# Performance work log

Measured on AMD Instinct MI355X. Metric: run time of the kernel, lower is better.

## Reference

```python
import jax, jax.numpy as jnp
import numpy as np

L = 2
NB = (L + 1) ** 2      # 9 spherical-harmonic basis components
C = 256                # in_channels == out_channels
MID = C // 4           # 64, mid_channels in the FF
N = 4096               # nodes
K = 16                 # neighbors (neighbor_cg)


def _real_sh_l2(rel):
    # Real spherical harmonics up to l=2 of normalized edge directions. rel: [N,K,3] -> [N,K,9]
    r = jnp.sqrt(jnp.sum(rel * rel, axis=-1, keepdims=True))
    d = rel / (r + 1e-8)
    x, y, z = d[..., 0], d[..., 1], d[..., 2]
    c0 = 0.28209479177387814
    c1 = 0.4886025119029199
    c2 = 1.0925484305920792
    c2b = 0.31539156525252005
    c2c = 0.5462742152960396
    return jnp.stack([
        jnp.full_like(x, c0),
        c1 * y, c1 * z, c1 * x,
        c2 * x * y, c2 * y * z, c2b * (3.0 * z * z - 1.0), c2 * x * z, c2c * (x * x - y * y),
    ], axis=-1)


def setup_inputs() -> dict:
    key = jax.random.key(0)
    ks = jax.random.split(key, 8)
    return {
        "s_feats": jax.random.normal(ks[0], (N, NB, C), jnp.float32),
        "s_points": jax.random.normal(ks[1], (N, 3), jnp.float32),
        "cg": jax.random.normal(ks[2], (NB, NB, NB), jnp.float32) * 0.1,  # CG coefficient buffer
        "W_proj": jax.random.normal(ks[3], (C, C), jnp.float32) / np.sqrt(C),
        "ln_w": jnp.ones((L + 1, C), jnp.float32),
        "ln_b": jnp.zeros((C,), jnp.float32),
        "W_ff1": jax.random.normal(ks[4], (C, MID), jnp.float32) / np.sqrt(C),
        "W_gate": jax.random.normal(ks[5], (MID, MID * (L + 1)), jnp.float32) / np.sqrt(MID),
        "W_ff2": jax.random.normal(ks[6], (MID, C), jnp.float32) / np.sqrt(MID),
        "neighbor_indices": jax.random.randint(ks[7], (N, K), 0, N),
    }


def _forward(s_feats, s_points, cg, W_proj, ln_w, ln_b, W_ff1, W_gate, W_ff2, neighbor_indices):
    # --- CGConv: project, gather neighbors, SH of edge directions, CG tensor product, mean-aggregate ---
    h = jnp.einsum('nic,co->nio', s_feats, W_proj)               # [N,9,C]
    nbr = h[neighbor_indices]                                    # [N,K,9,C] irregular gather
    rel = s_points[neighbor_indices] - s_points[:, None, :]      # [N,K,3]
    sh = _real_sh_l2(rel)                                        # [N,K,9]
    x = jnp.einsum('nkic,nkj,ijo->noc', nbr, sh, cg) / K         # [N,9,C]
    # --- residual add of input (linear3 == Identity since in_channels == out_channels) ---
    x = x + s_feats
    shortcut = x
    # --- EquivariantLayerNormV2: per-degree RMS norm; mean-center + bias only on l=0 ---
    outs = []
    for l in range(L + 1):
        f = x[:, l * l:(l + 1) * (l + 1), :]                     # [N,2l+1,C]
        if l == 0:
            f = f - jnp.mean(f, axis=-1, keepdims=True)
        nrm = jnp.mean(f * f, axis=(1, 2), keepdims=True)
        f = f * jax.lax.rsqrt(nrm + 1e-5) * ln_w[l][None, None, :]
        if l == 0:
            f = f + ln_b[None, None, :]
        outs.append(f)
    y = jnp.concatenate(outs, axis=1)
    # --- FF: Linear -> Gate_3j -> Linear, residual ---
    z = jnp.einsum('nic,cm->nim', y, W_ff1)                      # [N,9,MID]
    after = z[:, 0, :] @ W_gate                                  # [N, MID*(L+1)]
    t0 = jax.nn.silu(after[:, :MID])
    mult = jax.nn.sigmoid(after[:, MID:])                        # [N, MID*L]
    gated = [t0[:, None, :]]
    for l in range(1, L + 1):
        gated.append(z[:, l * l:(l + 1) * (l + 1), :] * mult[:, None, (l - 1) * MID:l * MID])
    z = jnp.concatenate(gated, axis=1)                           # [N,9,MID]
    return jnp.einsum('nim,mc->nic', z, W_ff2) + shortcut


def reference(s_feats, s_points, cg, W_proj, ln_w, ln_b, W_ff1, W_gate, W_ff2, neighbor_indices):
    return _forward(s_feats, s_points, cg, W_proj, ln_w, ln_b, W_ff1, W_gate, W_ff2, neighbor_indices)
```

## Files before the change

kernel.cpp:

```cpp
#include <hip/hip_runtime.h>
#include <hip/hip_bf16.h>

#define N_PTS  4096
#define NB     9
#define C      256
#define MID    64
#define KNBR   16
#define NROWS  (N_PTS * NB)

typedef __attribute__((ext_vector_type(8))) short          short8;
typedef __attribute__((ext_vector_type(4))) float          f32x4;
typedef __attribute__((ext_vector_type(4))) unsigned short ush4;
typedef __attribute__((ext_vector_type(8))) unsigned short ush8;

static __device__ __forceinline__ unsigned short f2bf(float f) {
    union { __hip_bfloat16 h; unsigned short u; } cv;
    cv.h = __float2bfloat16(f);
    return cv.u;
}
static __device__ __forceinline__ float bf2f(unsigned short s) {
    union { unsigned u; float f; } v; v.u = ((unsigned)s) << 16;
    return v.f;
}
static __device__ __forceinline__ unsigned packbf(float a, float b) {
    return (unsigned)f2bf(a) | ((unsigned)f2bf(b) << 16);
}

#define LDK 40
__global__ __launch_bounds__(256) void k_proj(const float* __restrict__ A,
                                              const float* __restrict__ W,
                                              unsigned short* __restrict__ H) {
    __shared__ unsigned short As[128 * LDK];
    __shared__ unsigned short Bs[128 * LDK];
    const int tid = threadIdx.x;
    const int r0  = blockIdx.x * 128;
    const int n0  = blockIdx.y * 128;
    const int wave = tid >> 6, lane = tid & 63;
    const int wm = wave >> 1, wn = wave & 1;
    const int lr = lane & 15, lg = lane >> 4;

    f32x4 acc[4][4];
#pragma unroll
    for (int a = 0; a < 4; ++a)
#pragma unroll
        for (int b = 0; b < 4; ++b) acc[a][b] = (f32x4){0.f, 0.f, 0.f, 0.f};

    for (int k0 = 0; k0 < C; k0 += 32) {
        __syncthreads();
#pragma unroll
        for (int rep = 0; rep < 4; ++rep) {
            const int e   = rep * 256 + tid;
            const int row = e >> 3;
            const int c4  = (e & 7) << 2;
            const float4 v = *reinterpret_cast<const float4*>(&A[(size_t)(r0 + row) * C + k0 + c4]);
            ush4 s = { f2bf(v.x), f2bf(v.y), f2bf(v.z), f2bf(v.w) };
            *reinterpret_cast<ush4*>(&As[row * LDK + c4]) = s;
        }
#pragma unroll
        for (int rep = 0; rep < 4; ++rep) {
            const int e = rep * 256 + tid;
            const int k = e >> 5;
            const int j = (e & 31) << 2;
            const float4 v = *reinterpret_cast<const float4*>(&W[(size_t)(k0 + k) * C + n0 + j]);
            Bs[(j + 0) * LDK + k] = f2bf(v.x);
            Bs[(j + 1) * LDK + k] = f2bf(v.y);
            Bs[(j + 2) * LDK + k] = f2bf(v.z);
            Bs[(j + 3) * LDK + k] = f2bf(v.w);
        }
        __syncthreads();

        short8 af[4], bfr[4];
#pragma unroll
        for (int mf = 0; mf < 4; ++mf)
            af[mf] = *reinterpret_cast<const short8*>(&As[(wm * 64 + mf * 16 + lr) * LDK + lg * 8]);
#pragma unroll
        for (int nf = 0; nf < 4; ++nf)
            bfr[nf] = *reinterpret_cast<const short8*>(&Bs[(wn * 64 + nf * 16 + lr) * LDK + lg * 8]);
#pragma unroll
        for (int mf = 0; mf < 4; ++mf)
#pragma unroll
            for (int nf = 0; nf < 4; ++nf)
                acc[mf][nf] = __builtin_amdgcn_mfma_f32_16x16x32_bf16(af[mf], bfr[nf], acc[mf][nf], 0, 0, 0);
    }
#pragma unroll
    for (int mf = 0; mf < 4; ++mf)
#pragma unroll
        for (int nf = 0; nf < 4; ++nf) {
            const int col = n0 + wn * 64 + nf * 16 + lr;
#pragma unroll
            for (int r = 0; r < 4; ++r) {
                const int row = r0 + wm * 64 + mf * 16 + lg * 4 + r;
                H[(size_t)row * C + col] = f2bf(acc[mf][nf][r]);
            }
        }
}

__global__ __launch_bounds__(256) void k_cg_ln(const unsigned short* __restrict__ Hb,
                                               const float* __restrict__ s_feats,
                                               const float* __restrict__ pts,
                                               const float* __restrict__ cg,
                                               const int*   __restrict__ nbr,
                                               const float* __restrict__ ln_w,
                                               const float* __restrict__ ln_b,
                                               unsigned short* __restrict__ Xb,
                                               unsigned short* __restrict__ Yb) {
    __shared__ unsigned short Bs[256 * 40];
    __shared__ unsigned short wT[16 * 168];
    __shared__ float cg_s[729];
    __shared__ float sh_s[KNBR][NB];
    __shared__ int   idx_s[KNBR];
    __shared__ float red_s[2][4];

    const int tid  = threadIdx.x;
    const int n    = blockIdx.x;
    const int wv   = tid >> 6;
    const int lane = tid & 63;
    const int g16  = lane >> 4;
    const int l16  = lane & 15;

    {
        unsigned* w32 = reinterpret_cast<unsigned*>(wT);
        for (int e = tid; e < (16 * 168) / 2; e += 256) w32[e] = 0u;
    }
    for (int e = tid; e < 729; e += 256) cg_s[e] = cg[e];
    if (tid < KNBR) {
        const int idx = nbr[n * KNBR + tid];
        idx_s[tid] = idx;
        const float px = pts[idx * 3 + 0] - pts[n * 3 + 0];
        const float py = pts[idx * 3 + 1] - pts[n * 3 + 1];
        const float pz = pts[idx * 3 + 2] - pts[n * 3 + 2];
        const float r  = sqrtf(px * px + py * py + pz * pz);
        const float iv = 1.f / (r + 1e-8f);
        const float dx = px * iv, dy = py * iv, dz = pz * iv;
        const float c1 = 0.4886025119029199f;
        const float c2 = 1.0925484305920792f;
        sh_s[tid][0] = 0.28209479177387814f;
        sh_s[tid][1] = c1 * dy;
        sh_s[tid][2] = c1 * dz;
        sh_s[tid][3] = c1 * dx;
        sh_s[tid][4] = c2 * dx * dy;
        sh_s[tid][5] = c2 * dy * dz;
        sh_s[tid][6] = 0.31539156525252005f * (3.f * dz * dz - 1.f);
        sh_s[tid][7] = c2 * dx * dz;
        sh_s[tid][8] = 0.5462742152960396f * (dx * dx - dy * dy);
    }
    __syncthreads();

    for (int t = tid; t < 144 * 9; t += 256) {
        const int ki = t / 9;
        const int o  = t - ki * 9;
        const int kk = ki / 9;
        const int ii = ki - kk * 9;
        float s = 0.f;
#pragma unroll
        for (int j = 0; j < 9; ++j) s = fmaf(sh_s[kk][j], cg_s[ii * 81 + j * 9 + o], s);
        wT[o * 168 + ki] = f2bf(s);
    }

    const int r = tid & 31;
    const int s = tid >> 5;

    f32x4 acc[4];
#pragma unroll
    for (int i = 0; i < 4; ++i) acc[i] = (f32x4){0.f, 0.f, 0.f, 0.f};

    for (int cc = 0; cc < 5; ++cc) {
        const int nrows = (cc == 4) ? 16 : 32;
        ush8 q[4];
        if (r < nrows) {
            const int ki = cc * 32 + r;
            const int kk = ki / 9;
            const int ii = ki - kk * 9;
            const unsigned short* hrow = Hb + (size_t)(idx_s[kk] * NB + ii) * C + s * 32;
#pragma unroll
            for (int u = 0; u < 4; ++u)
                q[u] = *reinterpret_cast<const ush8*>(hrow + u * 8);
        }
        __syncthreads();
        if (r < nrows) {
#pragma unroll
            for (int u = 0; u < 4; ++u) {
                const unsigned short* qe = reinterpret_cast<const unsigned short*>(&q[u]);
#pragma unroll
                for (int e = 0; e < 8; ++e)
                    Bs[(s * 32 + u * 8 + e) * 40 + r] = qe[e];
            }
        }
        __syncthreads();

        const short8 af = *reinterpret_cast<const short8*>(&wT[l16 * 168 + cc * 32 + g16 * 8]);
        short8 bfr[4];
#pragma unroll
        for (int ti = 0; ti < 4; ++ti)
            bfr[ti] = *reinterpret_cast<const short8*>(&Bs[(wv * 64 + ti * 16 + l16) * 40 + g16 * 8]);
#pragma unroll
        for (int ti = 0; ti < 4; ++ti)
            acc[ti] = __builtin_amdgcn_mfma_f32_16x16x32_bf16(af, bfr[ti], acc[ti], 0, 0, 0);
    }

    __syncthreads();
    float* const Dld = reinterpret_cast<float*>(Bs);
#pragma unroll
    for (int ti = 0; ti < 4; ++ti) {
        const int cgl = (wv * 4 + ti) * 16 + l16;
#pragma unroll
        for (int rr = 0; rr < 4; ++rr) {
            const int o = g16 * 4 + rr;
            if (o < 9) Dld[o * 264 + cgl] = acc[ti][rr] * (1.f / (float)KNBR);
        }
    }
    __syncthreads();

    float2 xv[9];
    float s0 = 0.f, s1 = 0.f, s2 = 0.f, s3 = 0.f;
    if (tid < 128) {
        const int c = tid * 2;
        const float* sf = s_feats + (size_t)n * (NB * C) + c;
#pragma unroll
        for (int i = 0; i < 9; ++i) {
            const float2 d = *reinterpret_cast<const float2*>(&Dld[i * 264 + c]);
            const float2 sv = *reinterpret_cast<const float2*>(&sf[(size_t)i * C]);
            xv[i].x = d.x + sv.x;
            xv[i].y = d.y + sv.y;
        }
        s0 = xv[0].x + xv[0].y;
        s1 = xv[0].x * xv[0].x + xv[0].y * xv[0].y;
#pragma unroll
        for (int o = 1; o < 4; ++o) s2 += xv[o].x * xv[o].x + xv[o].y * xv[o].y;
#pragma unroll
        for (int o = 4; o < 9; ++o) s3 += xv[o].x * xv[o].x + xv[o].y * xv[o].y;
#pragma unroll
        for (int off = 32; off >= 1; off >>= 1) {
            s0 += __shfl_xor(s0, off);
            s1 += __shfl_xor(s1, off);
            s2 += __shfl_xor(s2, off);
            s3 += __shfl_xor(s3, off);
        }
        if (lane == 0) {
            red_s[wv][0] = s0; red_s[wv][1] = s1;
            red_s[wv][2] = s2; red_s[wv][3] = s3;
        }
    }
    __syncthreads();
    if (tid < 128) {
        s0 = red_s[0][0] + red_s[1][0];
        s1 = red_s[0][1] + red_s[1][1];
        s2 = red_s[0][2] + red_s[1][2];
        s3 = red_s[0][3] + red_s[1][3];

        const float mean0 = s0 * (1.f / 256.f);
        const float nrm0  = s1 * (1.f / 256.f) - mean0 * mean0;
        const float nrm1  = s2 * (1.f / 768.f);
        const float nrm2  = s3 * (1.f / 1280.f);
        const float r0v = rsqrtf(nrm0 + 1e-5f);
        const float r1v = rsqrtf(nrm1 + 1e-5f);
        const float r2v = rsqrtf(nrm2 + 1e-5f);

        const int c = tid * 2;
        const float2 lw0 = *reinterpret_cast<const float2*>(ln_w + c);
        const float2 lw1 = *reinterpret_cast<const float2*>(ln_w + C + c);
        const float2 lw2 = *reinterpret_cast<const float2*>(ln_w + 2 * C + c);
        const float2 lb0 = *reinterpret_cast<const float2*>(ln_b + c);

        unsigned* xo = reinterpret_cast<unsigned*>(Xb + (size_t)n * (NB * C));
        unsigned* yo = reinterpret_cast<unsigned*>(Yb + (size_t)n * (NB * C));
#pragma unroll
        for (int i = 0; i < 9; ++i) xo[i * 128 + tid] = packbf(xv[i].x, xv[i].y);
        yo[tid] = packbf((xv[0].x - mean0) * r0v * lw0.x + lb0.x,
                         (xv[0].y - mean0) * r0v * lw0.y + lb0.y);
#pragma unroll
        for (int i = 1; i < 4; ++i)
            yo[i * 128 + tid] = packbf(xv[i].x * r1v * lw1.x, xv[i].y * r1v * lw1.y);
#pragma unroll
        for (int i = 4; i < 9; ++i)
            yo[i * 128 + tid] = packbf(xv[i].x * r2v * lw2.x, xv[i].y * r2v * lw2.y);
    }
}

__global__ __launch_bounds__(256) void k_ff1(const unsigned short* __restrict__ Yb,
                                             const float* __restrict__ W1,
                                             unsigned short* __restrict__ Zb) {
    __shared__ unsigned short As[128 * LDK];
    __shared__ unsigned short Bs[64 * LDK];
    const int tid = threadIdx.x;
    const int r0  = blockIdx.x * 128;
    const int wave = tid >> 6, lane = tid & 63;
    const int wm = wave >> 1, wn = wave & 1;
    const int lr = lane & 15, lg = lane >> 4;

    f32x4 acc[4][2];
#pragma unroll
    for (int a = 0; a < 4; ++a) { acc[a][0] = (f32x4){0.f,0.f,0.f,0.f}; acc[a][1] = (f32x4){0.f,0.f,0.f,0.f}; }

    for (int k0 = 0; k0 < C; k0 += 32) {
        __syncthreads();
#pragma unroll
        for (int rep = 0; rep < 4; ++rep) {
            const int e   = rep * 256 + tid;
            const int row = e >> 3;
            const int c4  = (e & 7) << 2;
            ush4 s = *reinterpret_cast<const ush4*>(&Yb[(size_t)(r0 + row) * C + k0 + c4]);
            *reinterpret_cast<ush4*>(&As[row * LDK + c4]) = s;
        }
#pragma unroll
        for (int rep = 0; rep < 2; ++rep) {
            const int e = rep * 256 + tid;
            const int k = e >> 4;
            const int j = (e & 15) << 2;
            const float4 v = *reinterpret_cast<const float4*>(&W1[(size_t)(k0 + k) * MID + j]);
            Bs[(j + 0) * LDK + k] = f2bf(v.x);
            Bs[(j + 1) * LDK + k] = f2bf(v.y);
            Bs[(j + 2) * LDK + k] = f2bf(v.z);
            Bs[(j + 3) * LDK + k] = f2bf(v.w);
        }
        __syncthreads();

        short8 af[4], bfr[2];
#pragma unroll
        for (int mf = 0; mf < 4; ++mf)
            af[mf] = *reinterpret_cast<const short8*>(&As[(wm * 64 + mf * 16 + lr) * LDK + lg * 8]);
#pragma unroll
        for (int nf = 0; nf < 2; ++nf)
            bfr[nf] = *reinterpret_cast<const short8*>(&Bs[(wn * 32 + nf * 16 + lr) * LDK + lg * 8]);
#pragma unroll
        for (int mf = 0; mf < 4; ++mf)
#pragma unroll
            for (int nf = 0; nf < 2; ++nf)
                acc[mf][nf] = __builtin_amdgcn_mfma_f32_16x16x32_bf16(af[mf], bfr[nf], acc[mf][nf], 0, 0, 0);
    }
#pragma unroll
    for (int mf = 0; mf < 4; ++mf)
#pragma unroll
        for (int nf = 0; nf < 2; ++nf) {
            const int col = wn * 32 + nf * 16 + lr;
#pragma unroll
            for (int r = 0; r < 4; ++r) {
                const int row = r0 + wm * 64 + mf * 16 + lg * 4 + r;
                Zb[(size_t)row * MID + col] = f2bf(acc[mf][nf][r]);
            }
        }
}

__global__ __launch_bounds__(192) void k_gate(const unsigned short* __restrict__ Zb,
                                              const float* __restrict__ Wg,
                                              float* __restrict__ G) {
    __shared__ float wgs[64 * 192];
    __shared__ float z0s[16 * 64];
    const int tid = threadIdx.x;
    const int n0  = blockIdx.x * 16;

    for (int e = tid; e < 64 * 192; e += 192) wgs[e] = Wg[e];
    for (int e = tid; e < 16 * 64; e += 192) {
        const int r = e >> 6, m = e & 63;
        z0s[e] = bf2f(Zb[(size_t)(n0 + r) * (NB * MID) + m]);
    }
    __syncthreads();

    const int j = tid;
    for (int r = 0; r < 16; ++r) {
        float acc = 0.f;
        for (int m0 = 0; m0 < 64; m0 += 4) {
            const float4 zv = *reinterpret_cast<const float4*>(&z0s[r * 64 + m0]);
            acc = fmaf(zv.x, wgs[(m0 + 0) * 192 + j], acc);
            acc = fmaf(zv.y, wgs[(m0 + 1) * 192 + j], acc);
            acc = fmaf(zv.z, wgs[(m0 + 2) * 192 + j], acc);
            acc = fmaf(zv.w, wgs[(m0 + 3) * 192 + j], acc);
        }
        const float sig = 1.f / (1.f + expf(-acc));
        G[(size_t)(n0 + r) * 192 + j] = (j < 64) ? acc * sig : sig;
    }
}

#define LDK64 72
__global__ __launch_bounds__(256) void k_final(const unsigned short* __restrict__ Zb,
                                               const float* __restrict__ G,
                                               const float* __restrict__ W2,
                                               const unsigned short* __restrict__ Xb,
                                               float* __restrict__ OUT) {
    __shared__ unsigned short As[128 * LDK64];
    __shared__ unsigned short Bs[128 * LDK64];
    const int tid = threadIdx.x;
    const int r0  = blockIdx.x * 128;
    const int n0  = blockIdx.y * 128;
    const int wave = tid >> 6, lane = tid & 63;
    const int wm = wave >> 1, wn = wave & 1;
    const int lr = lane & 15, lg = lane >> 4;

    {
        const int arow = tid >> 1;
        const int kh   = (tid & 1) * 32;
        const int grow = r0 + arow;
        const int nn   = grow / 9;
        const int ii   = grow - nn * 9;
        if (ii == 0) {
            const float* gp = &G[(size_t)nn * 192 + kh];
#pragma unroll
            for (int j = 0; j < 32; j += 4) {
                const float4 g = *reinterpret_cast<const float4*>(&gp[j]);
                ush4 s = { f2bf(g.x), f2bf(g.y), f2bf(g.z), f2bf(g.w) };
                *reinterpret_cast<ush4*>(&As[arow * LDK64 + kh + j]) = s;
            }
        } else {
            const float* gm = &G[(size_t)nn * 192 + ((ii < 4) ? 64 : 128) + kh];
            const unsigned short* zr = &Zb[(size_t)nn * (NB * MID) + ii * MID + kh];
#pragma unroll
            for (int j = 0; j < 32; j += 4) {
                const ush4 zv = *reinterpret_cast<const ush4*>(&zr[j]);
                const float4 g = *reinterpret_cast<const float4*>(&gm[j]);
                ush4 s = { f2bf(bf2f(zv.x) * g.x), f2bf(bf2f(zv.y) * g.y),
                           f2bf(bf2f(zv.z) * g.z), f2bf(bf2f(zv.w) * g.w) };
                *reinterpret_cast<ush4*>(&As[arow * LDK64 + kh + j]) = s;
            }
        }
    }
#pragma unroll
    for (int rep = 0; rep < 8; ++rep) {
        const int e = rep * 256 + tid;
        const int k = e >> 5;
        const int j = (e & 31) << 2;
        const float4 v = *reinterpret_cast<const float4*>(&W2[(size_t)k * C + n0 + j]);
        Bs[(j + 0) * LDK64 + k] = f2bf(v.x);
        Bs[(j + 1) * LDK64 + k] = f2bf(v.y);
        Bs[(j + 2) * LDK64 + k] = f2bf(v.z);
        Bs[(j + 3) * LDK64 + k] = f2bf(v.w);
    }
    __syncthreads();

    f32x4 acc[4][4];
#pragma unroll
    for (int a = 0; a < 4; ++a)
#pragma unroll
        for (int b = 0; b < 4; ++b) acc[a][b] = (f32x4){0.f, 0.f, 0.f, 0.f};

#pragma unroll
    for (int ks = 0; ks < 2; ++ks) {
        short8 af[4], bfr[4];
#pragma unroll
        for (int mf = 0; mf < 4; ++mf)
            af[mf] = *reinterpret_cast<const short8*>(&As[(wm * 64 + mf * 16 + lr) * LDK64 + ks * 32 + lg * 8]);
#pragma unroll
        for (int nf = 0; nf < 4; ++nf)
            bfr[nf] = *reinterpret_cast<const short8*>(&Bs[(wn * 64 + nf * 16 + lr) * LDK64 + ks * 32 + lg * 8]);
#pragma unroll
        for (int mf = 0; mf < 4; ++mf)
#pragma unroll
            for (int nf = 0; nf < 4; ++nf)
                acc[mf][nf] = __builtin_amdgcn_mfma_f32_16x16x32_bf16(af[mf], bfr[nf], acc[mf][nf], 0, 0, 0);
    }

#pragma unroll
    for (int mf = 0; mf < 4; ++mf)
#pragma unroll
        for (int nf = 0; nf < 4; ++nf) {
            const int col = n0 + wn * 64 + nf * 16 + lr;
#pragma unroll
            for (int r = 0; r < 4; ++r) {
                const int row = r0 + wm * 64 + mf * 16 + lg * 4 + r;
                OUT[(size_t)row * C + col] = acc[mf][nf][r] + bf2f(Xb[(size_t)row * C + col]);
            }
        }
}

extern "C" void kernel_launch(void* const* d_in, const int* in_sizes, int n_in,
                              void* d_out, int out_size, void* d_ws, size_t ws_size,
                              hipStream_t stream) {
    const float* s_feats = (const float*)d_in[0];
    const float* s_pts   = (const float*)d_in[1];
    const float* cg      = (const float*)d_in[2];
    const float* W_proj  = (const float*)d_in[3];
    const float* ln_w    = (const float*)d_in[4];
    const float* ln_b    = (const float*)d_in[5];
    const float* W_ff1   = (const float*)d_in[6];
    const float* W_gate  = (const float*)d_in[7];
    const float* W_ff2   = (const float*)d_in[8];
    const int*   nbr     = (const int*)d_in[9];
    float* out = (float*)d_out;

    unsigned short* Hb = (unsigned short*)d_ws;
    unsigned short* Xb = Hb + (size_t)NROWS * C;
    unsigned short* Yb = Xb + (size_t)NROWS * C;
    unsigned short* Zb = Yb + (size_t)NROWS * C;
    float* G = (float*)(Zb + (size_t)NROWS * MID);

    k_proj  <<<dim3(NROWS / 128, 2), 256, 0, stream>>>(s_feats, W_proj, Hb);
    k_cg_ln <<<N_PTS,                256, 0, stream>>>(Hb, s_feats, s_pts, cg, nbr, ln_w, ln_b, Xb, Yb);
    k_ff1   <<<NROWS / 128,          256, 0, stream>>>(Yb, W_ff1, Zb);
    k_gate  <<<N_PTS / 16,           192, 0, stream>>>(Zb, W_gate, G);
    k_final <<<dim3(NROWS / 128, 2), 256, 0, stream>>>(Zb, G, W_ff2, Xb, out);
}
```

Baseline: 131.9 us.

## Software-pipeline neighbor row gathers and alias CG coefficients into the staging buffer

The cg_ln kernel now issues the first chunk's neighbor-row gather before building the wT weight table, and prefetches the next chunk's rows into registers while the current chunk is written to shared memory and consumed by MFMA. The CG coefficient array no longer has its own shared-memory allocation and instead lives in the Bs staging buffer, lowering LDS use per block and possibly raising occupancy. The aim is to hide global gather latency behind compute. The cost is more live registers and a layout that depends on barrier ordering between the wT build and the first Bs write.

```diff
diff --git a/kernel.cpp b/kernel.cpp
--- a/kernel.cpp
+++ b/kernel.cpp
@@ -106,10 +106,11 @@
                                                unsigned short* __restrict__ Yb) {
     __shared__ unsigned short Bs[256 * 40];
     __shared__ unsigned short wT[16 * 168];
-    __shared__ float cg_s[729];
     __shared__ float sh_s[KNBR][NB];
     __shared__ int   idx_s[KNBR];
     __shared__ float red_s[2][4];
+
+    float* const cg_s = reinterpret_cast<float*>(Bs);
 
     const int tid  = threadIdx.x;
     const int n    = blockIdx.x;
@@ -146,19 +147,31 @@
     }
     __syncthreads();
 
+    const int r = tid & 31;
+    const int s = tid >> 5;
+
+    ush8 q0, q1, q2, q3;
+    {
+        const int ki = r;
+        const int kk = ki / 9;
+        const int ii = ki - kk * 9;
+        const unsigned short* hrow = Hb + (size_t)(idx_s[kk] * NB + ii) * C + s * 32;
+        q0 = *reinterpret_cast<const ush8*>(hrow + 0);
+        q1 = *reinterpret_cast<const ush8*>(hrow + 8);
+        q2 = *reinterpret_cast<const ush8*>(hrow + 16);
+        q3 = *reinterpret_cast<const ush8*>(hrow + 24);
+    }
+
     for (int t = tid; t < 144 * 9; t += 256) {
         const int ki = t / 9;
         const int o  = t - ki * 9;
         const int kk = ki / 9;
         const int ii = ki - kk * 9;
-        float s = 0.f;
-#pragma unroll
-        for (int j = 0; j < 9; ++j) s = fmaf(sh_s[kk][j], cg_s[ii * 81 + j * 9 + o], s);
-        wT[o * 168 + ki] = f2bf(s);
-    }
-
-    const int r = tid & 31;
-    const int s = tid >> 5;
+        float sv = 0.f;
+#pragma unroll
+        for (int j = 0; j < 9; ++j) sv = fmaf(sh_s[kk][j], cg_s[ii * 81 + j * 9 + o], sv);
+        wT[o * 168 + ki] = f2bf(sv);
+    }
 
     f32x4 acc[4];
 #pragma unroll
@@ -166,26 +179,39 @@
 
     for (int cc = 0; cc < 5; ++cc) {
         const int nrows = (cc == 4) ? 16 : 32;
-        ush8 q[4];
+
+        __syncthreads();
+
         if (r < nrows) {
-            const int ki = cc * 32 + r;
-            const int kk = ki / 9;
-            const int ii = ki - kk * 9;
-            const unsigned short* hrow = Hb + (size_t)(idx_s[kk] * NB + ii) * C + s * 32;
-#pragma unroll
-            for (int u = 0; u < 4; ++u)
-                q[u] = *reinterpret_cast<const ush8*>(hrow + u * 8);
-        }
-        __syncthreads();
-        if (r < nrows) {
-#pragma unroll
-            for (int u = 0; u < 4; ++u) {
-                const unsigned short* qe = reinterpret_cast<const unsigned short*>(&q[u]);
-#pragma unroll
-                for (int e = 0; e < 8; ++e)
-                    Bs[(s * 32 + u * 8 + e) * 40 + r] = qe[e];
+            const unsigned short* qe;
+            qe = reinterpret_cast<const unsigned short*>(&q0);
+#pragma unroll
+            for (int e = 0; e < 8; ++e) Bs[(s * 32 + 0 * 8 + e) * 40 + r] = qe[e];
+            qe = reinterpret_cast<const unsigned short*>(&q1);
+#pragma unroll
+            for (int e = 0; e < 8; ++e) Bs[(s * 32 + 1 * 8 + e) * 40 + r] = qe[e];
+            qe = reinterpret_cast<const unsigned short*>(&q2);
+#pragma unroll
+            for (int e = 0; e < 8; ++e) Bs[(s * 32 + 2 * 8 + e) * 40 + r] = qe[e];
+            qe = reinterpret_cast<const unsigned short*>(&q3);
+#pragma unroll
+            for (int e = 0; e < 8; ++e) Bs[(s * 32 + 3 * 8 + e) * 40 + r] = qe[e];
+        }
+
+        if (cc < 4) {
+            const int kin   = (cc + 1) * 32 + r;
+            const bool vldn = (kin < 144);
+            if (vldn) {
+                const int kk = kin / 9;
+                const int ii = kin - kk * 9;
+                const unsigned short* hrow = Hb + (size_t)(idx_s[kk] * NB + ii) * C + s * 32;
+                q0 = *reinterpret_cast<const ush8*>(hrow + 0);
+                q1 = *reinterpret_cast<const ush8*>(hrow + 8);
+                q2 = *reinterpret_cast<const ush8*>(hrow + 16);
+                q3 = *reinterpret_cast<const ush8*>(hrow + 24);
             }
         }
+
         __syncthreads();
 
         const short8 af = *reinterpret_cast<const short8*>(&wT[l16 * 168 + cc * 32 + g16 * 8]);
@@ -218,7 +244,7 @@
         const float* sf = s_feats + (size_t)n * (NB * C) + c;
 #pragma unroll
         for (int i = 0; i < 9; ++i) {
-            const float2 d = *reinterpret_cast<const float2*>(&Dld[i * 264 + c]);
+            const float2 d  = *reinterpret_cast<const float2*>(&Dld[i * 264 + c]);
             const float2 sv = *reinterpret_cast<const float2*>(&sf[(size_t)i * C]);
             xv[i].x = d.x + sv.x;
             xv[i].y = d.y + sv.y;
```

Measured after the change: 129.4 us. About the same (-1.9%).

## Split CG kernel by channel halves, precompute edge weights, fold layernorm into FF1

Applied to the files above, without the earlier changes.

The per-node CG-weight construction moves into a separate kernel that writes a bf16 weight matrix per node. The CG conv is split over two channel halves per node, and all neighbor rows are gathered in one pass into an XOR-swizzled LDS tile instead of a five-step load/sync loop. The layernorm is no longer a separate Y buffer: partial sums go to a scratch array and FF1 applies the normalization while loading X. This aims to raise parallelism, cut synchronizations and drop one full-size intermediate write and read, at the cost of an extra launch, a weight buffer round trip and recomputed norm statistics in FF1.

```diff
diff --git a/kernel.cpp b/kernel.cpp
--- a/kernel.cpp
+++ b/kernel.cpp
@@ -95,37 +95,18 @@
         }
 }
 
-__global__ __launch_bounds__(256) void k_cg_ln(const unsigned short* __restrict__ Hb,
-                                               const float* __restrict__ s_feats,
-                                               const float* __restrict__ pts,
-                                               const float* __restrict__ cg,
-                                               const int*   __restrict__ nbr,
-                                               const float* __restrict__ ln_w,
-                                               const float* __restrict__ ln_b,
-                                               unsigned short* __restrict__ Xb,
-                                               unsigned short* __restrict__ Yb) {
-    __shared__ unsigned short Bs[256 * 40];
-    __shared__ unsigned short wT[16 * 168];
+__global__ __launch_bounds__(256) void k_w(const float* __restrict__ pts,
+                                           const float* __restrict__ cg,
+                                           const int*   __restrict__ nbr,
+                                           unsigned short* __restrict__ w_all) {
     __shared__ float cg_s[729];
     __shared__ float sh_s[KNBR][NB];
-    __shared__ int   idx_s[KNBR];
-    __shared__ float red_s[2][4];
-
-    const int tid  = threadIdx.x;
-    const int n    = blockIdx.x;
-    const int wv   = tid >> 6;
-    const int lane = tid & 63;
-    const int g16  = lane >> 4;
-    const int l16  = lane & 15;
-
-    {
-        unsigned* w32 = reinterpret_cast<unsigned*>(wT);
-        for (int e = tid; e < (16 * 168) / 2; e += 256) w32[e] = 0u;
-    }
+    const int tid = threadIdx.x;
+    const int n   = blockIdx.x;
+
     for (int e = tid; e < 729; e += 256) cg_s[e] = cg[e];
     if (tid < KNBR) {
         const int idx = nbr[n * KNBR + tid];
-        idx_s[tid] = idx;
         const float px = pts[idx * 3 + 0] - pts[n * 3 + 0];
         const float py = pts[idx * 3 + 1] - pts[n * 3 + 1];
         const float pz = pts[idx * 3 + 2] - pts[n * 3 + 2];
@@ -146,85 +127,120 @@
     }
     __syncthreads();
 
-    for (int t = tid; t < 144 * 9; t += 256) {
-        const int ki = t / 9;
-        const int o  = t - ki * 9;
-        const int kk = ki / 9;
-        const int ii = ki - kk * 9;
+#pragma unroll
+    for (int it = 0; it < 10; ++it) {
+        const int t  = it * 256 + tid;
+        const int o  = t / 160;
+        const int ki = t - o * 160;
         float s = 0.f;
-#pragma unroll
-        for (int j = 0; j < 9; ++j) s = fmaf(sh_s[kk][j], cg_s[ii * 81 + j * 9 + o], s);
-        wT[o * 168 + ki] = f2bf(s);
-    }
-
-    const int r = tid & 31;
-    const int s = tid >> 5;
-
-    f32x4 acc[4];
-#pragma unroll
-    for (int i = 0; i < 4; ++i) acc[i] = (f32x4){0.f, 0.f, 0.f, 0.f};
-
-    for (int cc = 0; cc < 5; ++cc) {
-        const int nrows = (cc == 4) ? 16 : 32;
-        ush8 q[4];
-        if (r < nrows) {
-            const int ki = cc * 32 + r;
+        if (o < 9 && ki < 144) {
             const int kk = ki / 9;
             const int ii = ki - kk * 9;
-            const unsigned short* hrow = Hb + (size_t)(idx_s[kk] * NB + ii) * C + s * 32;
-#pragma unroll
-            for (int u = 0; u < 4; ++u)
-                q[u] = *reinterpret_cast<const ush8*>(hrow + u * 8);
-        }
-        __syncthreads();
-        if (r < nrows) {
-#pragma unroll
-            for (int u = 0; u < 4; ++u) {
-                const unsigned short* qe = reinterpret_cast<const unsigned short*>(&q[u]);
-#pragma unroll
-                for (int e = 0; e < 8; ++e)
-                    Bs[(s * 32 + u * 8 + e) * 40 + r] = qe[e];
-            }
-        }
-        __syncthreads();
-
-        const short8 af = *reinterpret_cast<const short8*>(&wT[l16 * 168 + cc * 32 + g16 * 8]);
-        short8 bfr[4];
-#pragma unroll
-        for (int ti = 0; ti < 4; ++ti)
-            bfr[ti] = *reinterpret_cast<const short8*>(&Bs[(wv * 64 + ti * 16 + l16) * 40 + g16 * 8]);
-#pragma unroll
-        for (int ti = 0; ti < 4; ++ti)
-            acc[ti] = __builtin_amdgcn_mfma_f32_16x16x32_bf16(af, bfr[ti], acc[ti], 0, 0, 0);
+#pragma unroll
+            for (int j = 0; j < 9; ++j) s = fmaf(sh_s[kk][j], cg_s[ii * 81 + j * 9 + o], s);
+        }
+        w_all[(size_t)n * 2560 + t] = f2bf(s);
+    }
+}
+
+__global__ __launch_bounds__(256) void k_cg(const unsigned short* __restrict__ Hb,
+                                            const float* __restrict__ s_feats,
+                                            const unsigned short* __restrict__ w_all,
+                                            const int*   __restrict__ nbr,
+                                            unsigned short* __restrict__ Xb,
+                                            float* __restrict__ scr) {
+    __shared__ unsigned short Bs[128 * 168];
+    __shared__ unsigned short wTl[16 * 168];
+    __shared__ int idx_s[KNBR];
+
+    const int tid  = threadIdx.x;
+    const int bid  = blockIdx.x;
+    const int n    = bid >> 1;
+    const int half = bid & 1;
+    const int c0   = half * 128;
+    const int wv   = tid >> 6;
+    const int lane = tid & 63;
+    const int g16  = lane >> 4;
+    const int l16  = lane & 15;
+
+    if (tid < KNBR) idx_s[tid] = nbr[n * KNBR + tid];
+    __syncthreads();
+
+    const int cseg = tid & 15;
+    const int kk   = tid >> 4;
+    const unsigned short* hb = Hb + (size_t)idx_s[kk] * (NB * C) + c0 + cseg * 8;
+    ush8 q[9];
+#pragma unroll
+    for (int j = 0; j < 9; ++j)
+        q[j] = *reinterpret_cast<const ush8*>(hb + (size_t)j * C);
+
+    {
+        const int u  = tid;
+        const int o  = u / 20, p = u - o * 20;
+        const ush8 wv8 = *reinterpret_cast<const ush8*>(w_all + (size_t)n * 2560 + o * 160 + p * 8);
+        *reinterpret_cast<ush8*>(&wTl[o * 168 + p * 8]) = wv8;
+        if (tid < 64) {
+            const int u2 = 256 + tid;
+            const int o2 = u2 / 20, p2 = u2 - o2 * 20;
+            const ush8 w2 = *reinterpret_cast<const ush8*>(w_all + (size_t)n * 2560 + o2 * 160 + p2 * 8);
+            *reinterpret_cast<ush8*>(&wTl[o2 * 168 + p2 * 8]) = w2;
+        }
+    }
+    if (tid < 128) {
+        const ush8 z = (ush8){0, 0, 0, 0, 0, 0, 0, 0};
+        *reinterpret_cast<ush8*>(&Bs[tid * 168 + 144]) = z;
+        *reinterpret_cast<ush8*>(&Bs[tid * 168 + 152]) = z;
+        *reinterpret_cast<ush8*>(&Bs[tid * 168 + 160]) = z;
+    }
+#pragma unroll
+    for (int j = 0; j < 9; ++j) {
+        const unsigned short* qe = reinterpret_cast<const unsigned short*>(&q[j]);
+        const int colk = kk * 9 + j;
+#pragma unroll
+        for (int e = 0; e < 8; ++e) {
+            const int ee = e ^ (cseg & 7);
+            Bs[(cseg * 8 + ee) * 168 + colk] = qe[ee];
+        }
+    }
+    __syncthreads();
+
+    f32x4 acc[2];
+    acc[0] = (f32x4){0.f, 0.f, 0.f, 0.f};
+    acc[1] = (f32x4){0.f, 0.f, 0.f, 0.f};
+#pragma unroll
+    for (int cc = 0; cc < 5; ++cc) {
+        const short8 af = *reinterpret_cast<const short8*>(&wTl[l16 * 168 + cc * 32 + g16 * 8]);
+        const short8 b0 = *reinterpret_cast<const short8*>(&Bs[(wv * 32 + l16) * 168 + cc * 32 + g16 * 8]);
+        const short8 b1 = *reinterpret_cast<const short8*>(&Bs[(wv * 32 + 16 + l16) * 168 + cc * 32 + g16 * 8]);
+        acc[0] = __builtin_amdgcn_mfma_f32_16x16x32_bf16(af, b0, acc[0], 0, 0, 0);
+        acc[1] = __builtin_amdgcn_mfma_f32_16x16x32_bf16(af, b1, acc[1], 0, 0, 0);
     }
 
     __syncthreads();
     float* const Dld = reinterpret_cast<float*>(Bs);
 #pragma unroll
-    for (int ti = 0; ti < 4; ++ti) {
-        const int cgl = (wv * 4 + ti) * 16 + l16;
+    for (int tt = 0; tt < 2; ++tt) {
+        const int cl = wv * 32 + tt * 16 + l16;
 #pragma unroll
         for (int rr = 0; rr < 4; ++rr) {
             const int o = g16 * 4 + rr;
-            if (o < 9) Dld[o * 264 + cgl] = acc[ti][rr] * (1.f / (float)KNBR);
-        }
-    }
-    __syncthreads();
-
-    float2 xv[9];
-    float s0 = 0.f, s1 = 0.f, s2 = 0.f, s3 = 0.f;
-    if (tid < 128) {
-        const int c = tid * 2;
-        const float* sf = s_feats + (size_t)n * (NB * C) + c;
+            if (o < 9) Dld[o * 132 + cl] = acc[tt][rr] * (1.f / (float)KNBR);
+        }
+    }
+    __syncthreads();
+
+    if (tid < 64) {
+        const int cl = tid * 2;
+        const float* sf = s_feats + (size_t)n * (NB * C) + c0 + cl;
+        float2 xv[9];
 #pragma unroll
         for (int i = 0; i < 9; ++i) {
-            const float2 d = *reinterpret_cast<const float2*>(&Dld[i * 264 + c]);
-            const float2 sv = *reinterpret_cast<const float2*>(&sf[(size_t)i * C]);
-            xv[i].x = d.x + sv.x;
-            xv[i].y = d.y + sv.y;
-        }
-        s0 = xv[0].x + xv[0].y;
-        s1 = xv[0].x * xv[0].x + xv[0].y * xv[0].y;
+            xv[i].x = Dld[i * 132 + cl]     + sf[(size_t)i * C];
+            xv[i].y = Dld[i * 132 + cl + 1] + sf[(size_t)i * C + 1];
+        }
+        float s0 = xv[0].x + xv[0].y;
+        float s1 = xv[0].x * xv[0].x + xv[0].y * xv[0].y;
+        float s2 = 0.f, s3 = 0.f;
 #pragma unroll
         for (int o = 1; o < 4; ++o) s2 += xv[o].x * xv[o].x + xv[o].y * xv[o].y;
 #pragma unroll
@@ -236,48 +252,20 @@
             s2 += __shfl_xor(s2, off);
             s3 += __shfl_xor(s3, off);
         }
-        if (lane == 0) {
-            red_s[wv][0] = s0; red_s[wv][1] = s1;
-            red_s[wv][2] = s2; red_s[wv][3] = s3;
-        }
-    }
-    __syncthreads();
-    if (tid < 128) {
-        s0 = red_s[0][0] + red_s[1][0];
-        s1 = red_s[0][1] + red_s[1][1];
-        s2 = red_s[0][2] + red_s[1][2];
-        s3 = red_s[0][3] + red_s[1][3];
-
-        const float mean0 = s0 * (1.f / 256.f);
-        const float nrm0  = s1 * (1.f / 256.f) - mean0 * mean0;
-        const float nrm1  = s2 * (1.f / 768.f);
-        const float nrm2  = s3 * (1.f / 1280.f);
-        const float r0v = rsqrtf(nrm0 + 1e-5f);
-        const float r1v = rsqrtf(nrm1 + 1e-5f);
-        const float r2v = rsqrtf(nrm2 + 1e-5f);
-
-        const int c = tid * 2;
-        const float2 lw0 = *reinterpret_cast<const float2*>(ln_w + c);
-        const float2 lw1 = *reinterpret_cast<const float2*>(ln_w + C + c);
-        const float2 lw2 = *reinterpret_cast<const float2*>(ln_w + 2 * C + c);
-        const float2 lb0 = *reinterpret_cast<const float2*>(ln_b + c);
-
-        unsigned* xo = reinterpret_cast<unsigned*>(Xb + (size_t)n * (NB * C));
-        unsigned* yo = reinterpret_cast<unsigned*>(Yb + (size_t)n * (NB * C));
+        unsigned* xo = reinterpret_cast<unsigned*>(Xb + (size_t)n * (NB * C) + c0);
 #pragma unroll
         for (int i = 0; i < 9; ++i) xo[i * 128 + tid] = packbf(xv[i].x, xv[i].y);
-        yo[tid] = packbf((xv[0].x - mean0) * r0v * lw0.x + lb0.x,
-                         (xv[0].y - mean0) * r0v * lw0.y + lb0.y);
-#pragma unroll
-        for (int i = 1; i < 4; ++i)
-            yo[i * 128 + tid] = packbf(xv[i].x * r1v * lw1.x, xv[i].y * r1v * lw1.y);
-#pragma unroll
-        for (int i = 4; i < 9; ++i)
-            yo[i * 128 + tid] = packbf(xv[i].x * r2v * lw2.x, xv[i].y * r2v * lw2.y);
-    }
-}
-
-__global__ __launch_bounds__(256) void k_ff1(const unsigned short* __restrict__ Yb,
+        if (tid == 0) {
+            float* sp = scr + (size_t)n * 8 + half * 4;
+            sp[0] = s0; sp[1] = s1; sp[2] = s2; sp[3] = s3;
+        }
+    }
+}
+
+__global__ __launch_bounds__(256) void k_ff1(const unsigned short* __restrict__ Xb,
+                                             const float* __restrict__ scr,
+                                             const float* __restrict__ ln_w,
+                                             const float* __restrict__ ln_b,
                                              const float* __restrict__ W1,
                                              unsigned short* __restrict__ Zb) {
     __shared__ unsigned short As[128 * LDK];
@@ -288,6 +276,28 @@
     const int wm = wave >> 1, wn = wave & 1;
     const int lr = lane & 15, lg = lane >> 4;
 
+    float mu_[4], rv_[4];
+    int   cls_[4];
+#pragma unroll
+    for (int rep = 0; rep < 4; ++rep) {
+        const int row = r0 + ((rep * 256 + tid) >> 3);
+        const int nn  = row / 9;
+        const int ii  = row - nn * 9;
+        const float* sp = scr + (size_t)nn * 8;
+        const float a0 = sp[0] + sp[4], a1 = sp[1] + sp[5];
+        const float a2 = sp[2] + sp[6], a3 = sp[3] + sp[7];
+        if (ii == 0) {
+            const float mu = a0 * (1.f / 256.f);
+            mu_[rep] = mu;
+            rv_[rep] = rsqrtf(a1 * (1.f / 256.f) - mu * mu + 1e-5f);
+            cls_[rep] = 0;
+        } else if (ii < 4) {
+            mu_[rep] = 0.f; rv_[rep] = rsqrtf(a2 * (1.f / 768.f) + 1e-5f); cls_[rep] = 1;
+        } else {
+            mu_[rep] = 0.f; rv_[rep] = rsqrtf(a3 * (1.f / 1280.f) + 1e-5f); cls_[rep] = 2;
+        }
+    }
+
     f32x4 acc[4][2];
 #pragma unroll
     for (int a = 0; a < 4; ++a) { acc[a][0] = (f32x4){0.f,0.f,0.f,0.f}; acc[a][1] = (f32x4){0.f,0.f,0.f,0.f}; }
@@ -299,7 +309,18 @@
             const int e   = rep * 256 + tid;
             const int row = e >> 3;
             const int c4  = (e & 7) << 2;
-            ush4 s = *reinterpret_cast<const ush4*>(&Yb[(size_t)(r0 + row) * C + k0 + c4]);
+            const ush4 xq = *reinterpret_cast<const ush4*>(&Xb[(size_t)(r0 + row) * C + k0 + c4]);
+            const float4 lw = *reinterpret_cast<const float4*>(&ln_w[cls_[rep] * C + k0 + c4]);
+            const float mu = mu_[rep], rv = rv_[rep];
+            float yx = (bf2f(xq.x) - mu) * rv * lw.x;
+            float yy = (bf2f(xq.y) - mu) * rv * lw.y;
+            float yz = (bf2f(xq.z) - mu) * rv * lw.z;
+            float yw = (bf2f(xq.w) - mu) * rv * lw.w;
+            if (cls_[rep] == 0) {
+                const float4 lb = *reinterpret_cast<const float4*>(&ln_b[k0 + c4]);
+                yx += lb.x; yy += lb.y; yz += lb.z; yw += lb.w;
+            }
+            ush4 s = { f2bf(yx), f2bf(yy), f2bf(yz), f2bf(yw) };
             *reinterpret_cast<ush4*>(&As[row * LDK + c4]) = s;
         }
 #pragma unroll
@@ -476,15 +497,17 @@
     const int*   nbr     = (const int*)d_in[9];
     float* out = (float*)d_out;
 
-    unsigned short* Hb = (unsigned short*)d_ws;
-    unsigned short* Xb = Hb + (size_t)NROWS * C;
-    unsigned short* Yb = Xb + (size_t)NROWS * C;
-    unsigned short* Zb = Yb + (size_t)NROWS * C;
-    float* G = (float*)(Zb + (size_t)NROWS * MID);
+    unsigned short* Hb    = (unsigned short*)d_ws;
+    unsigned short* Xb    = Hb + (size_t)NROWS * C;
+    unsigned short* Zb    = Xb + (size_t)NROWS * C;
+    unsigned short* w_all = Zb + (size_t)NROWS * MID;
+    float* G   = (float*)(w_all + (size_t)N_PTS * 2560);
+    float* scr = G + (size_t)N_PTS * 192;
 
     k_proj  <<<dim3(NROWS / 128, 2), 256, 0, stream>>>(s_feats, W_proj, Hb);
-    k_cg_ln <<<N_PTS,                256, 0, stream>>>(Hb, s_feats, s_pts, cg, nbr, ln_w, ln_b, Xb, Yb);
-    k_ff1   <<<NROWS / 128,          256, 0, stream>>>(Yb, W_ff1, Zb);
+    k_w     <<<N_PTS,                256, 0, stream>>>(s_pts, cg, nbr, w_all);
+    k_cg    <<<N_PTS * 2,            256, 0, stream>>>(Hb, s_feats, w_all, nbr, Xb, scr);
+    k_ff1   <<<NROWS / 128,          256, 0, stream>>>(Xb, scr, ln_w, ln_b, W_ff1, Zb);
     k_gate  <<<N_PTS / 16,           192, 0, stream>>>(Zb, W_gate, G);
     k_final <<<dim3(NROWS / 128, 2), 256, 0, stream>>>(Zb, G, W_ff2, Xb, out);
 }
```

Result: slower. 228.9 us (+73.5%).
